# Optimization experiments

Measured on AMD Instinct MI355X. Metric: run time of the kernel, lower is better.

The kernel has to match this reference:

```python
import jax, jax.numpy as jnp
import numpy as np

B, T, D, H = 2, 2048, 2048, 16
HD = D // H  # head_dim = 128
NEG = -1e9


def setup_inputs() -> dict:
    key = jax.random.key(0)
    k1, k2, k3 = jax.random.split(key, 3)
    x = jax.random.normal(k1, (B, T, D), dtype=jnp.float32)
    # additive causal mask: 0 on/below diagonal, large negative above
    mask = jnp.where(jnp.tril(jnp.ones((T, T), dtype=bool)), 0.0, NEG).astype(jnp.float32)
    causal_mask = mask[None, None]  # [1,1,T,T]
    w_qkv = jax.random.normal(k2, (3 * D, D), dtype=jnp.float32) * (D ** -0.5)
    w_out = jax.random.normal(k3, (D, D), dtype=jnp.float32) * (D ** -0.5)
    b_out = jnp.zeros((D,), dtype=jnp.float32)
    return {"x": x, "causal_mask": causal_mask, "w_qkv": w_qkv, "w_out": w_out, "b_out": b_out}


def reference(x, causal_mask, w_qkv, w_out, b_out):
    scale = HD ** -0.5
    qkv = jnp.einsum('btd,ed->bte', x, w_qkv)          # [B,T,3D]
    q, k, v = jnp.split(qkv, 3, axis=-1)
    def heads(t):  # [B,T,D] -> [B,H,T,HD]
        return t.reshape(B, T, H, HD).transpose(0, 2, 1, 3)
    q, k, v = heads(q), heads(k), heads(v)
    attn = jnp.einsum('bhqd,bhkd->bhqk', q, k) * scale + causal_mask
    attn = jax.nn.softmax(attn, axis=-1)
    out = jnp.einsum('bhqk,bhkd->bhqd', attn, v)       # [B,H,T,HD]
    out = out.transpose(0, 2, 1, 3).reshape(B, T, D)
    return jnp.einsum('btd,ed->bte', out, w_out) + b_out
```

## Files before the change

kernel.cpp:

```cpp
#include <hip/hip_runtime.h>
#include <stdint.h>

typedef uint16_t u16;
typedef __attribute__((ext_vector_type(8))) short short8;
typedef __attribute__((ext_vector_type(4))) float f32x4;
typedef __attribute__((ext_vector_type(16))) float f32x16;

#define MFMA16(a, b, c) __builtin_amdgcn_mfma_f32_16x16x32_bf16((a), (b), (c), 0, 0, 0)
#define MFMA32(a, b, c) __builtin_amdgcn_mfma_f32_32x32x16_bf16((a), (b), (c), 0, 0, 0)
#define AS1 __attribute__((address_space(1)))
#define AS3 __attribute__((address_space(3)))

__device__ __forceinline__ void gld_lds16(const u16* g, u16* l) {
  __builtin_amdgcn_global_load_lds((const AS1 void*)g, (AS3 void*)l, 16, 0, 0);
}

__device__ __forceinline__ u16 f2bf(float f) {
  uint32_t u = __float_as_uint(f);
  u += 0x7fffu + ((u >> 16) & 1u);
  return (u16)(u >> 16);
}

__global__ __launch_bounds__(256) void cvt_all(const float* __restrict__ x,
                                               const float* __restrict__ wqkv,
                                               const float* __restrict__ wout,
                                               u16* __restrict__ xb,
                                               u16* __restrict__ wqkvb,
                                               u16* __restrict__ woutb) {
  const int n1 = 8388608 / 4, n2 = 12582912 / 4;
  int i = blockIdx.x * 256 + threadIdx.x;
  const float* src;
  u16* dst;
  int j;
  if (i < n1) {
    src = x; dst = xb; j = i;
  } else if (i < n1 + n2) {
    src = wqkv; dst = wqkvb; j = i - n1;
  } else {
    src = wout; dst = woutb; j = i - n1 - n2;
  }
  float4 v = ((const float4*)src)[j];
  uint2 o;
  o.x = (uint32_t)f2bf(v.x) | ((uint32_t)f2bf(v.y) << 16);
  o.y = (uint32_t)f2bf(v.z) | ((uint32_t)f2bf(v.w) << 16);
  ((uint2*)dst)[j] = o;
}

template <int N>
__device__ __forceinline__ void bar_vm() {
  asm volatile("s_waitcnt vmcnt(%0)\n\ts_barrier" ::"n"(N) : "memory");
}
__device__ __forceinline__ void bar_fence() {
  asm volatile("s_barrier" ::: "memory");
}

__global__ __launch_bounds__(512, 2) void proj8_gemm(const u16* __restrict__ xb,
                                                     const u16* __restrict__ wqkvb,
                                                     u16* __restrict__ qkb) {
  constexpr int ASZ = 256 * 64;
  constexpr int NT = 32;
  __shared__ u16 sm[4 * ASZ];

  int bx = blockIdx.x;
  bx = (bx & 7) * 32 + (bx >> 3);
  const int mt = bx >> 4, nt = bx & 15;
  const u16* Ab = xb + (size_t)mt * 256 * 2048;
  const u16* Bb = wqkvb + (size_t)nt * 256 * 2048;
  u16* C = qkb + (size_t)mt * 256 * 4096 + nt * 256;

  const int tid = threadIdx.x, lane = tid & 63, w = tid >> 6;
  const int wm = w >> 2, wn = w & 3;
  const int lo = lane & 15, q4 = lane >> 4;

  f32x4 acc[8][4];
  const f32x4 fzero = {0.f, 0.f, 0.f, 0.f};
#pragma unroll
  for (int i = 0; i < 8; ++i)
#pragma unroll
    for (int j = 0; j < 4; ++j) acc[i][j] = fzero;

  auto stage_half = [&](int tau, int h) {
    const int slot = tau & 1;
    const int k0 = tau * 64;
    const u16* G = (h < 2) ? Bb : Ab;
    u16* L = sm + (h < 2 ? 2 * ASZ : 0) + slot * ASZ;
#pragma unroll
    for (int s = 0; s < 2; ++s) {
      const int c = tid + s * 512;
      const int hr = c >> 3, pc = c & 7;
      const int r = (h < 2) ? (h * 128 + hr)
                            : ((hr & 63) + ((hr >> 6) << 7) + ((h & 1) << 6));
      const int c4 = pc ^ (r & 7);
      gld_lds16(G + (size_t)r * 2048 + k0 + c4 * 8, L + r * 64 + pc * 8);
    }
  };

  stage_half(0, 0);
  stage_half(0, 1);
  stage_half(0, 2);
  stage_half(0, 3);
  bar_vm<2>();

  for (int tau = 0; tau < NT; ++tau) {
    const u16* As = sm + (tau & 1) * ASZ;
    const u16* Bs = sm + 2 * ASZ + (tau & 1) * ASZ;
    short8 bf[8];
#pragma unroll
    for (int q = 0; q < 4; ++q) {
      if (q == 0) {
#pragma unroll
        for (int j = 0; j < 4; ++j)
#pragma unroll
          for (int kk = 0; kk < 2; ++kk) {
            const int r = wn * 64 + j * 16 + lo;
            bf[j * 2 + kk] =
                *(const short8*)(Bs + r * 64 + (((kk * 4 + q4) ^ (r & 7)) * 8));
          }
      }
      short8 af[2][2];
#pragma unroll
      for (int i = 0; i < 2; ++i)
#pragma unroll
        for (int kk = 0; kk < 2; ++kk) {
          const int r = wm * 128 + q * 32 + i * 16 + lo;
          af[i][kk] =
              *(const short8*)(As + r * 64 + (((kk * 4 + q4) ^ (r & 7)) * 8));
        }
      if (tau + 1 < NT) stage_half(tau + 1, q);
      bar_fence();
      __builtin_amdgcn_s_setprio(1);
#pragma unroll
      for (int i = 0; i < 2; ++i)
#pragma unroll
        for (int j = 0; j < 4; ++j)
#pragma unroll
          for (int kk = 0; kk < 2; ++kk)
            acc[q * 2 + i][j] = MFMA16(af[i][kk], bf[j * 2 + kk], acc[q * 2 + i][j]);
      __builtin_amdgcn_s_setprio(0);
      if (q == 0) {
        if (tau == NT - 1) bar_vm<0>();
        else bar_vm<2>();
      } else if (q == 1) {
        bar_vm<4>();
      } else if (q == 2) {
        bar_vm<6>();
      } else {
        if (tau < NT - 1) bar_vm<2>();
      }
    }
  }

  const float sc =
      (nt < 8) ? (0.08838834764831843f * 1.4426950408889634f) : 1.0f;
#pragma unroll
  for (int i = 0; i < 8; ++i)
#pragma unroll
    for (int j = 0; j < 4; ++j) {
      const int col = wn * 64 + j * 16 + lo;
#pragma unroll
      for (int e = 0; e < 4; ++e) {
        const int row = wm * 128 + i * 16 + q4 * 4 + e;
        C[(size_t)row * 4096 + col] = f2bf(acc[i][j][e] * sc);
      }
    }
}

template <int MFR>
__device__ __forceinline__ void gemm_core3(const u16* __restrict__ Ab,
                                           const u16* __restrict__ Bb,
                                           u16* sm, int tid,
                                           f32x4 acc[MFR][4]) {
  constexpr int AROWS = MFR * 32;
  constexpr int ASZ = AROWS * 32;
  constexpr int BSZ = 128 * 32;
  constexpr int BUF = ASZ + BSZ;
  constexpr int NT = 64;
  constexpr int ALD = AROWS / 64;
  constexpr int VN = ALD + 2;

  const int lane = tid & 63, w = tid >> 6;
  const int wr = w >> 1, wc = w & 1;
  const int lo = lane & 15, q4 = lane >> 4;
  const int pcl = (((lo & 1) << 2) | q4) ^ ((lo >> 1) & 7);
  const int loff = (lo >> 1) * 64 + pcl * 8;

  auto stage = [&](int g) {
    u16* As = sm + (g % 3) * BUF;
    u16* Bs = As + ASZ;
    const int k0 = g * 32;
#pragma unroll
    for (int s = 0; s < ALD; ++s) {
      const int c = tid + s * 256;
      const int sr = c >> 3, pc = c & 7;
      const int t = pc ^ (sr & 7);
      const int r = sr * 2 + (t >> 2), c4 = t & 3;
      gld_lds16(Ab + (size_t)r * 2048 + k0 + c4 * 8, As + c * 8);
    }
#pragma unroll
    for (int s = 0; s < 2; ++s) {
      const int c = tid + s * 256;
      const int sr = c >> 3, pc = c & 7;
      const int t = pc ^ (sr & 7);
      const int r = sr * 2 + (t >> 2), c4 = t & 3;
      gld_lds16(Bb + (size_t)r * 2048 + k0 + c4 * 8, Bs + c * 8);
    }
  };

  stage(0);
  stage(1);
  bar_vm<VN>();

  for (int g = 0; g < NT; ++g) {
    const u16* As = sm + (g % 3) * BUF;
    const u16* Bs = As + ASZ;
    if (g + 2 < NT) stage(g + 2);
    short8 af[MFR], bf[4];
#pragma unroll
    for (int i = 0; i < MFR; ++i)
      af[i] = *(const short8*)(As + (wr * (MFR * 16) + i * 16) * 32 + loff);
#pragma unroll
    for (int j = 0; j < 4; ++j)
      bf[j] = *(const short8*)(Bs + (wc * 64 + j * 16) * 32 + loff);
    __builtin_amdgcn_s_setprio(1);
#pragma unroll
    for (int i = 0; i < MFR; ++i)
#pragma unroll
      for (int j = 0; j < 4; ++j) acc[i][j] = MFMA16(af[i], bf[j], acc[i][j]);
    __builtin_amdgcn_s_setprio(0);
    if (g + 1 < NT) {
      if (g + 2 < NT) {
        bar_vm<VN>();
      } else {
        bar_vm<0>();
      }
    }
  }
}

__global__ __launch_bounds__(256, 2) void vproj_gemm(const u16* __restrict__ wqkvb,
                                                     const u16* __restrict__ xb,
                                                     u16* __restrict__ vtb) {
  __shared__ u16 sm[3 * (128 * 32 + 128 * 32)];
  int bx = blockIdx.x;
  bx = (bx & 7) * 64 + (bx >> 3);
  const int tid = threadIdx.x;
  const int mt = bx >> 5, nt = bx & 31;
  const u16* Ab = wqkvb + (size_t)(4096 + mt * 128) * 2048;
  const u16* Bb = xb + (size_t)nt * 128 * 2048;
  u16* C = vtb + (size_t)mt * 128 * 4096 + nt * 128;
  f32x4 acc[4][4];
  const f32x4 fzero = {0.f, 0.f, 0.f, 0.f};
#pragma unroll
  for (int i = 0; i < 4; ++i)
#pragma unroll
    for (int j = 0; j < 4; ++j) acc[i][j] = fzero;

  gemm_core3<4>(Ab, Bb, sm, tid, acc);

  const int lane = tid & 63, w = tid >> 6;
  const int wr = w >> 1, wc = w & 1;
  const int lo = lane & 15, q4 = lane >> 4;
#pragma unroll
  for (int i = 0; i < 4; ++i)
#pragma unroll
    for (int j = 0; j < 4; ++j) {
      const int col = wc * 64 + j * 16 + lo;
#pragma unroll
      for (int e = 0; e < 4; ++e) {
        const int row = wr * 64 + i * 16 + q4 * 4 + e;
        C[(size_t)row * 4096 + col] = f2bf(acc[i][j][e]);
      }
    }
}

__global__ __launch_bounds__(256, 2) void out_gemm(const u16* __restrict__ A,
                                                   const u16* __restrict__ B,
                                                   float* __restrict__ Cf,
                                                   const float* __restrict__ bias) {
  __shared__ u16 sm[3 * (128 * 32 + 128 * 32)];
  int bx = blockIdx.x;
  bx = (bx & 7) * 64 + (bx >> 3);
  const int tid = threadIdx.x;
  const int mt = bx >> 4, nt = bx & 15;
  const u16* Ab = A + (size_t)mt * 128 * 2048;
  const u16* Bb = B + (size_t)nt * 128 * 2048;
  f32x4 acc[4][4];
  const f32x4 fzero = {0.f, 0.f, 0.f, 0.f};
#pragma unroll
  for (int i = 0; i < 4; ++i)
#pragma unroll
    for (int j = 0; j < 4; ++j) acc[i][j] = fzero;

  gemm_core3<4>(Ab, Bb, sm, tid, acc);

  const int lane = tid & 63, w = tid >> 6;
  const int wr = w >> 1, wc = w & 1;
  const int lo = lane & 15, q4 = lane >> 4;
#pragma unroll
  for (int i = 0; i < 4; ++i)
#pragma unroll
    for (int j = 0; j < 4; ++j) {
      const int col = nt * 128 + wc * 64 + j * 16 + lo;
      const float bv = bias[col];
#pragma unroll
      for (int e = 0; e < 4; ++e) {
        const int row = mt * 128 + wr * 64 + i * 16 + q4 * 4 + e;
        Cf[(size_t)row * 2048 + col] = acc[i][j][e] + bv;
      }
    }
}

__device__ __forceinline__ int swz(int r, int c) {
  return r * 128 + (c ^ (((r ^ (r >> 3)) & 7) << 4));
}

__global__ __launch_bounds__(512) void flash_attn(const u16* __restrict__ qk,
                                                  const u16* __restrict__ vt,
                                                  u16* __restrict__ aout) {
  constexpr int T = 2048, WQK = 4096, D = 2048;
  constexpr int TILE = 128 * 128;
  __shared__ u16 smem[4 * TILE];

  const int bx = blockIdx.x;
  const int p = bx >> 5;
  const int g = bx & 31;
  const int h = g & 15, b = g >> 4;
  const int tid = threadIdx.x, lane = tid & 63, w = tid >> 6;
  const int wr = w & 3, wk = w >> 2;
  const int l31 = lane & 31, hi = lane >> 5;

  const u16* Qb = qk + (size_t)b * T * WQK + h * 128;
  const u16* Kb = Qb + 2048;
  const u16* Vtb = vt + (size_t)h * 128 * 4096 + b * 2048;
  float* fex = (float*)smem;

  for (int half = 0; half < 2; ++half) {
    const int qt = half ? p : 15 - p;
    const int q0 = qt * 128;

    short8 qf[8];
#pragma unroll
    for (int kc = 0; kc < 8; ++kc)
      qf[kc] = *(const short8*)(Qb + (size_t)(q0 + wr * 32 + l31) * WQK +
                                kc * 16 + hi * 8);

    f32x16 o[4];
    float osum = 0.f;
#pragma unroll
    for (int dt = 0; dt < 4; ++dt)
#pragma unroll
      for (int e = 0; e < 16; ++e) o[dt][e] = 0.f;

    __syncthreads();
#pragma unroll
    for (int s = 0; s < 4; ++s) {
      const int c = tid + s * 512, r = c >> 4, cc = c & 15;
      const int cs = cc ^ (((r ^ (r >> 3)) & 7) << 1);
      gld_lds16(Kb + (size_t)r * WQK + cs * 8, smem + c * 8);
      gld_lds16(Vtb + (size_t)r * 4096 + cs * 8, smem + 2 * TILE + c * 8);
    }

    for (int kt = 0; kt <= qt; ++kt) {
      const int curo = (kt & 1) * TILE, nxto = TILE - curo;
      __syncthreads();
      if (kt < qt) {
        const int k0n = (kt + 1) * 128;
#pragma unroll
        for (int s = 0; s < 4; ++s) {
          const int c = tid + s * 512, r = c >> 4, cc = c & 15;
          const int cs = cc ^ (((r ^ (r >> 3)) & 7) << 1);
          gld_lds16(Kb + (size_t)(k0n + r) * WQK + cs * 8, smem + nxto + c * 8);
          gld_lds16(Vtb + (size_t)r * 4096 + k0n + cs * 8,
                    smem + 2 * TILE + nxto + c * 8);
        }
      }

      const u16* Ksc = smem + curo;
      const u16* Vsc = smem + 2 * TILE + curo;

      f32x16 s2[2];
#pragma unroll
      for (int e = 0; e < 16; ++e) { s2[0][e] = 0.f; s2[1][e] = 0.f; }
#pragma unroll
      for (int kc = 0; kc < 8; ++kc)
#pragma unroll
        for (int ct = 0; ct < 2; ++ct) {
          short8 kf = *(const short8*)&Ksc[swz(wk * 64 + ct * 32 + l31,
                                               kc * 16 + hi * 8)];
          s2[ct] = MFMA32(kf, qf[kc], s2[ct]);
        }

      const bool diag = (kt == qt);
#pragma unroll
      for (int ct = 0; ct < 2; ++ct) {
        float pv[16];
#pragma unroll
        for (int r = 0; r < 16; ++r) {
          float e = exp2f(s2[ct][r]);
          if (diag) {
            const int kcol = wk * 64 + ct * 32 + (r & 3) + 8 * (r >> 2) + 4 * hi;
            const int qrow = wr * 32 + l31;
            if (kcol > qrow) e = 0.f;
          }
          pv[r] = e;
          osum += e;
        }
        short8 pa2[2];
#pragma unroll
        for (int ks2 = 0; ks2 < 2; ++ks2) {
          uint32_t y0, y1, y2, y3;
          asm("v_cvt_pk_bf16_f32 %0, %1, %2"
              : "=v"(y0) : "v"(pv[ks2 * 8 + 0]), "v"(pv[ks2 * 8 + 1]));
          asm("v_cvt_pk_bf16_f32 %0, %1, %2"
              : "=v"(y1) : "v"(pv[ks2 * 8 + 2]), "v"(pv[ks2 * 8 + 3]));
          asm("v_cvt_pk_bf16_f32 %0, %1, %2"
              : "=v"(y2) : "v"(pv[ks2 * 8 + 4]), "v"(pv[ks2 * 8 + 5]));
          asm("v_cvt_pk_bf16_f32 %0, %1, %2"
              : "=v"(y3) : "v"(pv[ks2 * 8 + 6]), "v"(pv[ks2 * 8 + 7]));
          asm volatile("v_permlane32_swap_b32 %0, %1" : "+v"(y0), "+v"(y2));
          asm volatile("v_permlane32_swap_b32 %0, %1" : "+v"(y1), "+v"(y3));
          int4 t4;
          t4.x = (int)y0; t4.y = (int)y1; t4.z = (int)y2; t4.w = (int)y3;
          pa2[ks2] = *(short8*)&t4;
        }
#pragma unroll
        for (int ks2 = 0; ks2 < 2; ++ks2) {
          const int ksg = ct * 2 + ks2;
#pragma unroll
          for (int dt = 0; dt < 4; ++dt) {
            short8 vf = *(const short8*)&Vsc[swz(dt * 32 + l31,
                                                 wk * 64 + ksg * 16 + hi * 8)];
            o[dt] = MFMA32(pa2[ks2], vf, o[dt]);
          }
        }
      }
    }

    const float osum_full = osum + __shfl_xor(osum, 32);
    __syncthreads();
    if (wk == 1) {
#pragma unroll
      for (int dt = 0; dt < 4; ++dt)
#pragma unroll
        for (int r = 0; r < 16; ++r) {
          const int qr = wr * 32 + (r & 3) + 8 * (r >> 2) + 4 * hi;
          fex[qr * 128 + dt * 32 + l31] = o[dt][r];
        }
    }
    if (hi == 0) fex[16384 + wk * 128 + wr * 32 + l31] = osum_full;
    __syncthreads();
    if (wk == 0) {
#pragma unroll
      for (int r = 0; r < 16; ++r) {
        const int qr = wr * 32 + (r & 3) + 8 * (r >> 2) + 4 * hi;
        const float st = fex[16384 + qr] + fex[16384 + 128 + qr];
        const float inv = 1.f / st;
#pragma unroll
        for (int dt = 0; dt < 4; ++dt) {
          const float v = o[dt][r] + fex[qr * 128 + dt * 32 + l31];
          aout[(size_t)(b * T + q0 + qr) * D + h * 128 + dt * 32 + l31] =
              f2bf(v * inv);
        }
      }
    }
  }
}

extern "C" void kernel_launch(void* const* d_in, const int* in_sizes, int n_in,
                              void* d_out, int out_size, void* d_ws, size_t ws_size,
                              hipStream_t stream) {
  const float* x = (const float*)d_in[0];
  const float* w_qkv = (const float*)d_in[2];
  const float* w_out = (const float*)d_in[3];
  const float* b_out = (const float*)d_in[4];
  float* out = (float*)d_out;

  const int BT = 4096, D = 2048, D3 = 6144;
  u16* xb = (u16*)d_ws;
  u16* wqkvb = xb + (size_t)BT * D;
  u16* woutb = wqkvb + (size_t)D3 * D;
  u16* qkb = woutb + (size_t)D * D;
  u16* vtb = qkb + (size_t)BT * 4096;
  u16* attnb = vtb + (size_t)D * BT;

  const int total4 = (BT * D + D3 * D + D * D) / 4;
  cvt_all<<<total4 / 256, 256, 0, stream>>>(x, w_qkv, w_out, xb, wqkvb, woutb);
  proj8_gemm<<<256, 512, 0, stream>>>(xb, wqkvb, qkb);
  vproj_gemm<<<512, 256, 0, stream>>>(wqkvb, xb, vtb);
  flash_attn<<<256, 512, 0, stream>>>(qkb, vtb, attnb);
  out_gemm<<<512, 256, 0, stream>>>(attnb, woutb, out, b_out);
}
```

Before: 338.4 us.

## Split flash attention into one q-tile per block with 64-row KV tiles

The attention kernel stops pairing two q-tiles per block and launches one block per q-tile, doubling the grid. Halving the KV tile from 128 to 64 rows and using a simpler XOR swizzle cuts LDS use to about 66KB, so more blocks can share a CU. The launch bounds now request 4 blocks per CU to raise occupancy and overlap between blocks. The cost is a tighter register budget with possible spills, more barriers per unit of work, and loss of the explicit per-block causal load balancing.

```diff
diff --git a/kernel.cpp b/kernel.cpp
--- a/kernel.cpp
+++ b/kernel.cpp
@@ -310,21 +310,18 @@
     }
 }
 
-__device__ __forceinline__ int swz(int r, int c) {
-  return r * 128 + (c ^ (((r ^ (r >> 3)) & 7) << 4));
-}
-
-__global__ __launch_bounds__(512) void flash_attn(const u16* __restrict__ qk,
-                                                  const u16* __restrict__ vt,
-                                                  u16* __restrict__ aout) {
+__global__ __launch_bounds__(512, 4) void flash_attn(const u16* __restrict__ qk,
+                                                     const u16* __restrict__ vt,
+                                                     u16* __restrict__ aout) {
   constexpr int T = 2048, WQK = 4096, D = 2048;
-  constexpr int TILE = 128 * 128;
-  __shared__ u16 smem[4 * TILE];
+  constexpr int KT = 64 * 128;
+  __shared__ u16 smem[4 * KT + 512];
 
   const int bx = blockIdx.x;
-  const int p = bx >> 5;
   const int g = bx & 31;
   const int h = g & 15, b = g >> 4;
+  const int qt = (bx < 256) ? (bx >> 5) : (15 - ((bx - 256) >> 5));
+  const int q0 = qt * 128;
   const int tid = threadIdx.x, lane = tid & 63, w = tid >> 6;
   const int wr = w & 3, wk = w >> 2;
   const int l31 = lane & 31, hi = lane >> 5;
@@ -334,133 +331,127 @@
   const u16* Vtb = vt + (size_t)h * 128 * 4096 + b * 2048;
   float* fex = (float*)smem;
 
-  for (int half = 0; half < 2; ++half) {
-    const int qt = half ? p : 15 - p;
-    const int q0 = qt * 128;
-
-    short8 qf[8];
-#pragma unroll
-    for (int kc = 0; kc < 8; ++kc)
-      qf[kc] = *(const short8*)(Qb + (size_t)(q0 + wr * 32 + l31) * WQK +
-                                kc * 16 + hi * 8);
-
-    f32x16 o[4];
-    float osum = 0.f;
+  short8 qf[8];
+#pragma unroll
+  for (int kc = 0; kc < 8; ++kc)
+    qf[kc] = *(const short8*)(Qb + (size_t)(q0 + wr * 32 + l31) * WQK +
+                              kc * 16 + hi * 8);
+
+  f32x16 o[4];
+  float osum = 0.f;
+#pragma unroll
+  for (int dt = 0; dt < 4; ++dt)
+#pragma unroll
+    for (int e = 0; e < 16; ++e) o[dt][e] = 0.f;
+
+  auto stage = [&](int kt) {
+    const int kv0 = kt * 64;
+    u16* Kl = smem + (kt & 1) * KT;
+    u16* Vl = smem + 2 * KT + (kt & 1) * KT;
+#pragma unroll
+    for (int s = 0; s < 2; ++s) {
+      const int c = tid + s * 512;
+      {
+        const int r = c >> 4, pc = c & 15;
+        const int gc = pc ^ (r & 7);
+        gld_lds16(Kb + (size_t)(kv0 + r) * WQK + gc * 8, Kl + c * 8);
+      }
+      {
+        const int r = c >> 3, pc = c & 7;
+        const int gc = pc ^ (r & 7);
+        gld_lds16(Vtb + (size_t)r * 4096 + kv0 + gc * 8, Vl + c * 8);
+      }
+    }
+  };
+
+  stage(0);
+  const int ktmax = 2 * qt + 1;
+  for (int kt = 0; kt <= ktmax; ++kt) {
+    __syncthreads();
+    if (kt < ktmax) stage(kt + 1);
+    const u16* Ksc = smem + (kt & 1) * KT;
+    const u16* Vsc = smem + 2 * KT + (kt & 1) * KT;
+
+    f32x16 s2;
+#pragma unroll
+    for (int e = 0; e < 16; ++e) s2[e] = 0.f;
+    const int rk = wk * 32 + l31;
+#pragma unroll
+    for (int kc = 0; kc < 8; ++kc) {
+      short8 kf =
+          *(const short8*)&Ksc[rk * 128 + (((kc * 2 + hi) ^ (rk & 7)) * 8)];
+      s2 = MFMA32(kf, qf[kc], s2);
+    }
+
+    const bool diag = (kt >= 2 * qt);
+    float pv[16];
+#pragma unroll
+    for (int r = 0; r < 16; ++r) {
+      float e = exp2f(s2[r]);
+      if (diag) {
+        const int kcol = kt * 64 + wk * 32 + (r & 3) + 8 * (r >> 2) + 4 * hi;
+        const int qrow = q0 + wr * 32 + l31;
+        if (kcol > qrow) e = 0.f;
+      }
+      pv[r] = e;
+      osum += e;
+    }
+
+    short8 pa2[2];
+#pragma unroll
+    for (int ks2 = 0; ks2 < 2; ++ks2) {
+      uint32_t y0, y1, y2, y3;
+      asm("v_cvt_pk_bf16_f32 %0, %1, %2"
+          : "=v"(y0) : "v"(pv[ks2 * 8 + 0]), "v"(pv[ks2 * 8 + 1]));
+      asm("v_cvt_pk_bf16_f32 %0, %1, %2"
+          : "=v"(y1) : "v"(pv[ks2 * 8 + 2]), "v"(pv[ks2 * 8 + 3]));
+      asm("v_cvt_pk_bf16_f32 %0, %1, %2"
+          : "=v"(y2) : "v"(pv[ks2 * 8 + 4]), "v"(pv[ks2 * 8 + 5]));
+      asm("v_cvt_pk_bf16_f32 %0, %1, %2"
+          : "=v"(y3) : "v"(pv[ks2 * 8 + 6]), "v"(pv[ks2 * 8 + 7]));
+      asm volatile("v_permlane32_swap_b32 %0, %1" : "+v"(y0), "+v"(y2));
+      asm volatile("v_permlane32_swap_b32 %0, %1" : "+v"(y1), "+v"(y3));
+      int4 t4;
+      t4.x = (int)y0; t4.y = (int)y1; t4.z = (int)y2; t4.w = (int)y3;
+      pa2[ks2] = *(short8*)&t4;
+    }
+
+#pragma unroll
+    for (int ks2 = 0; ks2 < 2; ++ks2) {
+#pragma unroll
+      for (int dt = 0; dt < 4; ++dt) {
+        const int rv = dt * 32 + l31;
+        short8 vf = *(const short8*)&Vsc[rv * 64 +
+                                         (((wk * 4 + ks2 * 2 + hi) ^ (rv & 7)) * 8)];
+        o[dt] = MFMA32(pa2[ks2], vf, o[dt]);
+      }
+    }
+  }
+
+  const float osum_full = osum + __shfl_xor(osum, 32);
+  __syncthreads();
+  if (wk == 1) {
 #pragma unroll
     for (int dt = 0; dt < 4; ++dt)
-#pragma unroll
-      for (int e = 0; e < 16; ++e) o[dt][e] = 0.f;
-
-    __syncthreads();
-#pragma unroll
-    for (int s = 0; s < 4; ++s) {
-      const int c = tid + s * 512, r = c >> 4, cc = c & 15;
-      const int cs = cc ^ (((r ^ (r >> 3)) & 7) << 1);
-      gld_lds16(Kb + (size_t)r * WQK + cs * 8, smem + c * 8);
-      gld_lds16(Vtb + (size_t)r * 4096 + cs * 8, smem + 2 * TILE + c * 8);
-    }
-
-    for (int kt = 0; kt <= qt; ++kt) {
-      const int curo = (kt & 1) * TILE, nxto = TILE - curo;
-      __syncthreads();
-      if (kt < qt) {
-        const int k0n = (kt + 1) * 128;
-#pragma unroll
-        for (int s = 0; s < 4; ++s) {
-          const int c = tid + s * 512, r = c >> 4, cc = c & 15;
-          const int cs = cc ^ (((r ^ (r >> 3)) & 7) << 1);
-          gld_lds16(Kb + (size_t)(k0n + r) * WQK + cs * 8, smem + nxto + c * 8);
-          gld_lds16(Vtb + (size_t)r * 4096 + k0n + cs * 8,
-                    smem + 2 * TILE + nxto + c * 8);
-        }
-      }
-
-      const u16* Ksc = smem + curo;
-      const u16* Vsc = smem + 2 * TILE + curo;
-
-      f32x16 s2[2];
-#pragma unroll
-      for (int e = 0; e < 16; ++e) { s2[0][e] = 0.f; s2[1][e] = 0.f; }
-#pragma unroll
-      for (int kc = 0; kc < 8; ++kc)
-#pragma unroll
-        for (int ct = 0; ct < 2; ++ct) {
-          short8 kf = *(const short8*)&Ksc[swz(wk * 64 + ct * 32 + l31,
-                                               kc * 16 + hi * 8)];
-          s2[ct] = MFMA32(kf, qf[kc], s2[ct]);
-        }
-
-      const bool diag = (kt == qt);
-#pragma unroll
-      for (int ct = 0; ct < 2; ++ct) {
-        float pv[16];
-#pragma unroll
-        for (int r = 0; r < 16; ++r) {
-          float e = exp2f(s2[ct][r]);
-          if (diag) {
-            const int kcol = wk * 64 + ct * 32 + (r & 3) + 8 * (r >> 2) + 4 * hi;
-            const int qrow = wr * 32 + l31;
-            if (kcol > qrow) e = 0.f;
-          }
-          pv[r] = e;
-          osum += e;
-        }
-        short8 pa2[2];
-#pragma unroll
-        for (int ks2 = 0; ks2 < 2; ++ks2) {
-          uint32_t y0, y1, y2, y3;
-          asm("v_cvt_pk_bf16_f32 %0, %1, %2"
-              : "=v"(y0) : "v"(pv[ks2 * 8 + 0]), "v"(pv[ks2 * 8 + 1]));
-          asm("v_cvt_pk_bf16_f32 %0, %1, %2"
-              : "=v"(y1) : "v"(pv[ks2 * 8 + 2]), "v"(pv[ks2 * 8 + 3]));
-          asm("v_cvt_pk_bf16_f32 %0, %1, %2"
-              : "=v"(y2) : "v"(pv[ks2 * 8 + 4]), "v"(pv[ks2 * 8 + 5]));
-          asm("v_cvt_pk_bf16_f32 %0, %1, %2"
-              : "=v"(y3) : "v"(pv[ks2 * 8 + 6]), "v"(pv[ks2 * 8 + 7]));
-          asm volatile("v_permlane32_swap_b32 %0, %1" : "+v"(y0), "+v"(y2));
-          asm volatile("v_permlane32_swap_b32 %0, %1" : "+v"(y1), "+v"(y3));
-          int4 t4;
-          t4.x = (int)y0; t4.y = (int)y1; t4.z = (int)y2; t4.w = (int)y3;
-          pa2[ks2] = *(short8*)&t4;
-        }
-#pragma unroll
-        for (int ks2 = 0; ks2 < 2; ++ks2) {
-          const int ksg = ct * 2 + ks2;
-#pragma unroll
-          for (int dt = 0; dt < 4; ++dt) {
-            short8 vf = *(const short8*)&Vsc[swz(dt * 32 + l31,
-                                                 wk * 64 + ksg * 16 + hi * 8)];
-            o[dt] = MFMA32(pa2[ks2], vf, o[dt]);
-          }
-        }
-      }
-    }
-
-    const float osum_full = osum + __shfl_xor(osum, 32);
-    __syncthreads();
-    if (wk == 1) {
-#pragma unroll
-      for (int dt = 0; dt < 4; ++dt)
-#pragma unroll
-        for (int r = 0; r < 16; ++r) {
-          const int qr = wr * 32 + (r & 3) + 8 * (r >> 2) + 4 * hi;
-          fex[qr * 128 + dt * 32 + l31] = o[dt][r];
-        }
-    }
-    if (hi == 0) fex[16384 + wk * 128 + wr * 32 + l31] = osum_full;
-    __syncthreads();
-    if (wk == 0) {
 #pragma unroll
       for (int r = 0; r < 16; ++r) {
         const int qr = wr * 32 + (r & 3) + 8 * (r >> 2) + 4 * hi;
-        const float st = fex[16384 + qr] + fex[16384 + 128 + qr];
-        const float inv = 1.f / st;
-#pragma unroll
-        for (int dt = 0; dt < 4; ++dt) {
-          const float v = o[dt][r] + fex[qr * 128 + dt * 32 + l31];
-          aout[(size_t)(b * T + q0 + qr) * D + h * 128 + dt * 32 + l31] =
-              f2bf(v * inv);
-        }
+        fex[qr * 128 + dt * 32 + l31] = o[dt][r];
+      }
+  }
+  if (hi == 0) fex[16384 + wk * 128 + wr * 32 + l31] = osum_full;
+  __syncthreads();
+  if (wk == 0) {
+#pragma unroll
+    for (int r = 0; r < 16; ++r) {
+      const int qr = wr * 32 + (r & 3) + 8 * (r >> 2) + 4 * hi;
+      const float st = fex[16384 + qr] + fex[16384 + 128 + qr];
+      const float inv = 1.f / st;
+#pragma unroll
+      for (int dt = 0; dt < 4; ++dt) {
+        const float v = o[dt][r] + fex[qr * 128 + dt * 32 + l31];
+        aout[(size_t)(b * T + q0 + qr) * D + h * 128 + dt * 32 + l31] =
+            f2bf(v * inv);
       }
     }
   }
@@ -487,6 +478,6 @@
   cvt_all<<<total4 / 256, 256, 0, stream>>>(x, w_qkv, w_out, xb, wqkvb, woutb);
   proj8_gemm<<<256, 512, 0, stream>>>(xb, wqkvb, qkb);
   vproj_gemm<<<512, 256, 0, stream>>>(wqkvb, xb, vtb);
-  flash_attn<<<256, 512, 0, stream>>>(qkb, vtb, attnb);
+  flash_attn<<<512, 512, 0, stream>>>(qkb, vtb, attnb);
   out_gemm<<<512, 256, 0, stream>>>(attnb, woutb, out, b_out);
 }
```

After: 412.3 us. 21.8% more time.
